# Kernel tuning notes

Hardware: AMD Instinct MI355X
Metric: run time of the kernel (lower is better)

## Reference

```python
import jax, jax.numpy as jnp
import numpy as np

STRIDES = (8, 16, 32, 64, 128)
POOL = 7
IMG = 1024.0


def _crop_and_resize(fm, boxes, box_ids, crop_h, crop_w):
    """tf.image.crop_and_resize semantics (bilinear, extrapolation_value=0).
    fm: [B,H,W,C] channels-last; boxes: [N,4] normalized (y1,x1,y2,x2); box_ids: [N] int.
    Returns [N,crop_h,crop_w,C]."""
    B, H, W, C = fm.shape
    y1, x1, y2, x2 = boxes[:, 0], boxes[:, 1], boxes[:, 2], boxes[:, 3]
    fy = jnp.arange(crop_h, dtype=boxes.dtype) / (crop_h - 1)
    fx = jnp.arange(crop_w, dtype=boxes.dtype) / (crop_w - 1)
    ys = (y1[:, None] + (y2 - y1)[:, None] * fy) * (H - 1)   # [N,crop_h]
    xs = (x1[:, None] + (x2 - x1)[:, None] * fx) * (W - 1)   # [N,crop_w]
    y0f = jnp.floor(ys)
    x0f = jnp.floor(xs)
    wy = (ys - y0f)[:, :, None, None]
    wx = (xs - x0f)[:, None, :, None]
    y0 = jnp.clip(y0f, 0, H - 1).astype(jnp.int32)
    y1i = jnp.clip(y0f + 1, 0, H - 1).astype(jnp.int32)
    x0 = jnp.clip(x0f, 0, W - 1).astype(jnp.int32)
    x1i = jnp.clip(x0f + 1, 0, W - 1).astype(jnp.int32)
    b = box_ids[:, None, None]
    gather = lambda yi, xi: fm[b, yi[:, :, None], xi[:, None, :]]  # [N,ch,cw,C]
    top = gather(y0, x0) * (1 - wx) + gather(y0, x1i) * wx
    bot = gather(y1i, x0) * (1 - wx) + gather(y1i, x1i) * wx
    out = top * (1 - wy) + bot * wy
    valid = ((ys >= 0) & (ys <= H - 1))[:, :, None] & ((xs >= 0) & (xs <= W - 1))[:, None, :]
    return jnp.where(valid[..., None], out, jnp.zeros((), out.dtype))


def reference(batch_gt_boxes, fm0, fm1, fm2, fm3, fm4):
    boxes = batch_gt_boxes[..., :4]
    B, N, _ = boxes.shape
    box_ids = jnp.repeat(jnp.arange(B, dtype=jnp.int32), N)  # [B*N]
    boxes = boxes.reshape(-1, 4)
    # trim_padding_boxes: inputs contain no all-zero (padding) boxes, so all kept.
    rois_from_fms = []
    for fm, s in zip((fm0, fm1, fm2, fm3, fm4), STRIDES):
        H, W = fm.shape[1], fm.shape[2]
        # normalize_boxes: pixel coords -> feature-map coords (/stride) -> [0,1]
        scale = jnp.array([s * (H - 1), s * (W - 1), s * (H - 1), s * (W - 1)],
                          dtype=boxes.dtype)
        normed = boxes / scale
        rois_from_fms.append(_crop_and_resize(fm, normed, box_ids, POOL, POOL))
    rois = jnp.concatenate(rois_from_fms, axis=-1)  # [B*N, 7, 7, 5*C]
    return rois, box_ids


def setup_inputs() -> dict:
    key = jax.random.key(0)
    ks = jax.random.split(key, 6)
    u = jax.random.uniform(ks[0], (8, 100, 4), dtype=jnp.float32) * IMG
    ya, xa, yb, xb = u[..., 0], u[..., 1], u[..., 2], u[..., 3]
    # valid, non-degenerate, non-zero boxes (so trim_padding_boxes keeps all)
    batch_gt_boxes = jnp.stack([
        jnp.minimum(ya, yb), jnp.minimum(xa, xb),
        jnp.maximum(ya, yb) + 1.0, jnp.maximum(xa, xb) + 1.0], axis=-1)
    fms = {}
    for i, s in enumerate(STRIDES):
        hw = int(IMG) // s
        fms[f"fm{i}"] = jax.random.normal(ks[i + 1], (8, hw, hw, 256), dtype=jnp.float32)
    return {"batch_gt_boxes": batch_gt_boxes, **fms}
```

## Files before the change

### kernel.cpp

```cpp
#include <hip/hip_runtime.h>

#define NCH 256
#define ROIS_ELEMS 50176000

typedef float vf4 __attribute__((ext_vector_type(4)));

__global__ __launch_bounds__(256) void roi_row_kernel(
    const float* __restrict__ boxes,
    const float* __restrict__ fm0,
    const float* __restrict__ fm1,
    const float* __restrict__ fm2,
    const float* __restrict__ fm3,
    const float* __restrict__ fm4,
    float* __restrict__ out,
    float* __restrict__ out_ids)
{
    const int wave = threadIdx.x >> 6;
    const int lane = threadIdx.x & 63;

    const int bswz = (blockIdx.x & 7) * 875 + (blockIdx.x >> 3);
    const int row  = bswz * 4 + wave;

    const int n   = row / 35;
    const int rem = row - n * 35;
    const int l   = rem / 7;
    const int py  = rem - l * 7;

    const float* fm;
    switch (l) {
        case 0: fm = fm0; break;
        case 1: fm = fm1; break;
        case 2: fm = fm2; break;
        case 3: fm = fm3; break;
        default: fm = fm4; break;
    }
    const int H = 128 >> l;
    const float Hm1 = (float)(H - 1);
    const float scale = (float)((8 << l) * (H - 1));

    const int img = n / 100;
    const float y1 = boxes[n * 4 + 0];
    const float x1 = boxes[n * 4 + 1];
    const float y2 = boxes[n * 4 + 2];
    const float x2 = boxes[n * 4 + 3];

    const float y1n = __fdiv_rn(y1, scale);
    const float y2n = __fdiv_rn(y2, scale);
    const float x1n = __fdiv_rn(x1, scale);
    const float x2n = __fdiv_rn(x2, scale);

    const float fy = __fdiv_rn((float)py, 6.0f);
    const float ys = __fmul_rn(__fadd_rn(y1n, __fmul_rn(__fsub_rn(y2n, y1n), fy)), Hm1);
    const bool  vy = (ys >= 0.0f) && (ys <= Hm1);
    const float y0f = floorf(ys);
    const float wy  = ys - y0f;
    const float owy = 1.0f - wy;
    const int y0  = (int)fminf(fmaxf(y0f,        0.0f), Hm1);
    const int y1i = (int)fminf(fmaxf(y0f + 1.0f, 0.0f), Hm1);

    const int rowTop = (img * H + y0 ) * H;
    const int rowBot = (img * H + y1i) * H;

    float wx_[7];
    bool  vx_[7];
    int oT0[7], oT1[7], oB0[7], oB1[7];
    #pragma unroll
    for (int px = 0; px < 7; ++px) {
        const float fx = __fdiv_rn((float)px, 6.0f);
        const float xs = __fmul_rn(__fadd_rn(x1n, __fmul_rn(__fsub_rn(x2n, x1n), fx)), Hm1);
        vx_[px] = (xs >= 0.0f) && (xs <= Hm1);
        const float x0f = floorf(xs);
        wx_[px] = xs - x0f;
        const int x0  = (int)fminf(fmaxf(x0f,        0.0f), Hm1);
        const int x1i = (int)fminf(fmaxf(x0f + 1.0f, 0.0f), Hm1);
        oT0[px] = __builtin_amdgcn_readfirstlane((rowTop + x0 ) * NCH);
        oT1[px] = __builtin_amdgcn_readfirstlane((rowTop + x1i) * NCH);
        oB0[px] = __builtin_amdgcn_readfirstlane((rowBot + x0 ) * NCH);
        oB1[px] = __builtin_amdgcn_readfirstlane((rowBot + x1i) * NCH);
    }

    vf4 v00[7], v01[7], v10[7], v11[7];
    #pragma unroll
    for (int px = 0; px < 7; ++px) {
        v00[px] = ((const vf4*)(fm + oT0[px]))[lane];
        v01[px] = ((const vf4*)(fm + oT1[px]))[lane];
        v10[px] = ((const vf4*)(fm + oB0[px]))[lane];
        v11[px] = ((const vf4*)(fm + oB1[px]))[lane];
    }

    float* obase = out + ((n * 7 + py) * 7) * 1280 + l * NCH;
    #pragma unroll
    for (int px = 0; px < 7; ++px) {
        const float wx  = wx_[px];
        const float owx = 1.0f - wx;
        vf4 r = (v00[px] * owx + v01[px] * wx) * owy
              + (v10[px] * owx + v11[px] * wx) * wy;
        if (!(vy && vx_[px])) { r = (vf4)0.0f; }
        ((vf4*)(obase + px * 1280))[lane] = r;
    }

    if (l == 0 && py == 0 && lane == 0) {
        out_ids[n] = (float)img;
    }
}

extern "C" void kernel_launch(void* const* d_in, const int* in_sizes, int n_in,
                              void* d_out, int out_size, void* d_ws, size_t ws_size,
                              hipStream_t stream) {
    const float* boxes = (const float*)d_in[0];
    const float* fm0   = (const float*)d_in[1];
    const float* fm1   = (const float*)d_in[2];
    const float* fm2   = (const float*)d_in[3];
    const float* fm3   = (const float*)d_in[4];
    const float* fm4   = (const float*)d_in[5];

    float* out     = (float*)d_out;
    float* out_ids = out + ROIS_ELEMS;

    roi_row_kernel<<<7000, 256, 0, stream>>>(boxes, fm0, fm1, fm2, fm3, fm4, out, out_ids);
}
```

Measured before the change: 82.46 us.

## Remap waves to output cells covering all five levels with nontemporal stores

Each wave now handles one (box, py, px) output cell and loops over the five pyramid levels, instead of one (box, level, py) row covering seven px. Every wave therefore writes one contiguous 5 KB output chunk rather than seven strided 1 KB pieces, and the output stores become nontemporal so they skip the cache. The cost is redundant coordinate math across waves and more blocks. Gather reuse also changes: neighbouring px in the old scheme often shared source pixels within one wave.

```diff
diff --git a/kernel.cpp b/kernel.cpp
--- a/kernel.cpp
+++ b/kernel.cpp
@@ -5,7 +5,7 @@
 
 typedef float vf4 __attribute__((ext_vector_type(4)));
 
-__global__ __launch_bounds__(256) void roi_row_kernel(
+__global__ __launch_bounds__(256) void roi_cell_kernel(
     const float* __restrict__ boxes,
     const float* __restrict__ fm0,
     const float* __restrict__ fm1,
@@ -18,25 +18,15 @@
     const int wave = threadIdx.x >> 6;
     const int lane = threadIdx.x & 63;
 
-    const int bswz = (blockIdx.x & 7) * 875 + (blockIdx.x >> 3);
-    const int row  = bswz * 4 + wave;
+    const int bswz = (blockIdx.x & 7) * 1225 + (blockIdx.x >> 3);
+    const int cell = bswz * 4 + wave;
 
-    const int n   = row / 35;
-    const int rem = row - n * 35;
-    const int l   = rem / 7;
-    const int py  = rem - l * 7;
+    const int n   = cell / 49;
+    const int rem = cell - n * 49;
+    const int py  = rem / 7;
+    const int px  = rem - py * 7;
 
-    const float* fm;
-    switch (l) {
-        case 0: fm = fm0; break;
-        case 1: fm = fm1; break;
-        case 2: fm = fm2; break;
-        case 3: fm = fm3; break;
-        default: fm = fm4; break;
-    }
-    const int H = 128 >> l;
-    const float Hm1 = (float)(H - 1);
-    const float scale = (float)((8 << l) * (H - 1));
+    const float* fms[5] = { fm0, fm1, fm2, fm3, fm4 };
 
     const int img = n / 100;
     const float y1 = boxes[n * 4 + 0];
@@ -44,62 +34,65 @@
     const float y2 = boxes[n * 4 + 2];
     const float x2 = boxes[n * 4 + 3];
 
-    const float y1n = __fdiv_rn(y1, scale);
-    const float y2n = __fdiv_rn(y2, scale);
-    const float x1n = __fdiv_rn(x1, scale);
-    const float x2n = __fdiv_rn(x2, scale);
+    const float fy = __fdiv_rn((float)py, 6.0f);
+    const float fx = __fdiv_rn((float)px, 6.0f);
 
-    const float fy = __fdiv_rn((float)py, 6.0f);
-    const float ys = __fmul_rn(__fadd_rn(y1n, __fmul_rn(__fsub_rn(y2n, y1n), fy)), Hm1);
-    const bool  vy = (ys >= 0.0f) && (ys <= Hm1);
-    const float y0f = floorf(ys);
-    const float wy  = ys - y0f;
-    const float owy = 1.0f - wy;
-    const int y0  = (int)fminf(fmaxf(y0f,        0.0f), Hm1);
-    const int y1i = (int)fminf(fmaxf(y0f + 1.0f, 0.0f), Hm1);
+    float wy_[5], owy_[5], wx_[5], owx_[5];
+    bool  vv_[5];
+    int o00[5], o01[5], o10[5], o11[5];
+    #pragma unroll
+    for (int l = 0; l < 5; ++l) {
+        const int   H    = 128 >> l;
+        const float Hm1  = (float)(H - 1);
+        const float scale = (float)((8 << l) * (H - 1));
 
-    const int rowTop = (img * H + y0 ) * H;
-    const int rowBot = (img * H + y1i) * H;
+        const float y1n = __fdiv_rn(y1, scale);
+        const float y2n = __fdiv_rn(y2, scale);
+        const float x1n = __fdiv_rn(x1, scale);
+        const float x2n = __fdiv_rn(x2, scale);
 
-    float wx_[7];
-    bool  vx_[7];
-    int oT0[7], oT1[7], oB0[7], oB1[7];
-    #pragma unroll
-    for (int px = 0; px < 7; ++px) {
-        const float fx = __fdiv_rn((float)px, 6.0f);
+        const float ys = __fmul_rn(__fadd_rn(y1n, __fmul_rn(__fsub_rn(y2n, y1n), fy)), Hm1);
         const float xs = __fmul_rn(__fadd_rn(x1n, __fmul_rn(__fsub_rn(x2n, x1n), fx)), Hm1);
-        vx_[px] = (xs >= 0.0f) && (xs <= Hm1);
+        vv_[l] = (ys >= 0.0f) && (ys <= Hm1) && (xs >= 0.0f) && (xs <= Hm1);
+
+        const float y0f = floorf(ys);
         const float x0f = floorf(xs);
-        wx_[px] = xs - x0f;
+        wy_[l] = ys - y0f;  owy_[l] = 1.0f - wy_[l];
+        wx_[l] = xs - x0f;  owx_[l] = 1.0f - wx_[l];
+
+        const int y0  = (int)fminf(fmaxf(y0f,        0.0f), Hm1);
+        const int y1i = (int)fminf(fmaxf(y0f + 1.0f, 0.0f), Hm1);
         const int x0  = (int)fminf(fmaxf(x0f,        0.0f), Hm1);
         const int x1i = (int)fminf(fmaxf(x0f + 1.0f, 0.0f), Hm1);
-        oT0[px] = __builtin_amdgcn_readfirstlane((rowTop + x0 ) * NCH);
-        oT1[px] = __builtin_amdgcn_readfirstlane((rowTop + x1i) * NCH);
-        oB0[px] = __builtin_amdgcn_readfirstlane((rowBot + x0 ) * NCH);
-        oB1[px] = __builtin_amdgcn_readfirstlane((rowBot + x1i) * NCH);
+
+        const int rowT = (img * H + y0 ) * H;
+        const int rowB = (img * H + y1i) * H;
+        o00[l] = __builtin_amdgcn_readfirstlane((rowT + x0 ) * NCH);
+        o01[l] = __builtin_amdgcn_readfirstlane((rowT + x1i) * NCH);
+        o10[l] = __builtin_amdgcn_readfirstlane((rowB + x0 ) * NCH);
+        o11[l] = __builtin_amdgcn_readfirstlane((rowB + x1i) * NCH);
     }
 
-    vf4 v00[7], v01[7], v10[7], v11[7];
+    vf4 v00[5], v01[5], v10[5], v11[5];
     #pragma unroll
-    for (int px = 0; px < 7; ++px) {
-        v00[px] = ((const vf4*)(fm + oT0[px]))[lane];
-        v01[px] = ((const vf4*)(fm + oT1[px]))[lane];
-        v10[px] = ((const vf4*)(fm + oB0[px]))[lane];
-        v11[px] = ((const vf4*)(fm + oB1[px]))[lane];
+    for (int l = 0; l < 5; ++l) {
+        const float* fm = fms[l];
+        v00[l] = ((const vf4*)(fm + o00[l]))[lane];
+        v01[l] = ((const vf4*)(fm + o01[l]))[lane];
+        v10[l] = ((const vf4*)(fm + o10[l]))[lane];
+        v11[l] = ((const vf4*)(fm + o11[l]))[lane];
     }
 
-    float* obase = out + ((n * 7 + py) * 7) * 1280 + l * NCH;
+    float* obase = out + cell * 1280;
     #pragma unroll
-    for (int px = 0; px < 7; ++px) {
-        const float wx  = wx_[px];
-        const float owx = 1.0f - wx;
-        vf4 r = (v00[px] * owx + v01[px] * wx) * owy
-              + (v10[px] * owx + v11[px] * wx) * wy;
-        if (!(vy && vx_[px])) { r = (vf4)0.0f; }
-        ((vf4*)(obase + px * 1280))[lane] = r;
+    for (int l = 0; l < 5; ++l) {
+        vf4 r = (v00[l] * owx_[l] + v01[l] * wx_[l]) * owy_[l]
+              + (v10[l] * owx_[l] + v11[l] * wx_[l]) * wy_[l];
+        if (!vv_[l]) { r = (vf4)0.0f; }
+        __builtin_nontemporal_store(r, ((vf4*)(obase + l * NCH)) + lane);
     }
 
-    if (l == 0 && py == 0 && lane == 0) {
+    if (rem == 0 && lane == 0) {
         out_ids[n] = (float)img;
     }
 }
@@ -117,5 +110,5 @@
     float* out     = (float*)d_out;
     float* out_ids = out + ROIS_ELEMS;
 
-    roi_row_kernel<<<7000, 256, 0, stream>>>(boxes, fm0, fm1, fm2, fm3, fm4, out, out_ids);
+    roi_cell_kernel<<<9800, 256, 0, stream>>>(boxes, fm0, fm1, fm2, fm3, fm4, out, out_ids);
 }
```

Result: faster. 66.09 us (-19.9%).
